# Performance work log

Hardware: AMD Instinct MI355X
Metric: run time of the kernel (lower is better)

Reference implementation:

```python
import jax, jax.numpy as jnp
import numpy as np

E = 1024  # embed_dim
H = 16    # num_heads
D = E // H  # head_dim
B, S = 2, 2048

def _xavier(key, shape):
    fan_in, fan_out = shape[1], shape[0]
    limit = float(np.sqrt(6.0 / (fan_in + fan_out)))
    return jax.random.uniform(key, shape, jnp.float32, -limit, limit)

def setup_inputs() -> dict:
    key = jax.random.key(0)
    ks = jax.random.split(key, 7)
    return {
        "query": jax.random.normal(ks[0], (B, S, E), jnp.float32),
        "key": jax.random.normal(ks[1], (B, S, E), jnp.float32),
        "value": jax.random.normal(ks[2], (B, S, E), jnp.float32),
        "Wq": _xavier(ks[3], (E, E)), "bq": jnp.zeros((E,), jnp.float32),
        "Wk": _xavier(ks[4], (E, E)), "bk": jnp.zeros((E,), jnp.float32),
        "Wv": _xavier(ks[5], (E, E)), "bv": jnp.zeros((E,), jnp.float32),
        "Wo": _xavier(ks[6], (E, E)), "bo": jnp.zeros((E,), jnp.float32),
    }

def reference(query, key, value, Wq, bq, Wk, bk, Wv, bv, Wo, bo):
    b, s, e = query.shape
    # nn.Linear: x @ W^T + b
    Q = (query @ Wq.T + bq).reshape(b, s, H, D).transpose(0, 2, 1, 3)  # [b,h,s,d]
    K = (key @ Wk.T + bk).reshape(b, s, H, D).transpose(0, 2, 1, 3)
    V = (value @ Wv.T + bv).reshape(b, s, H, D).transpose(0, 2, 1, 3)
    scale = D ** -0.5
    scores = jnp.einsum('bhqd,bhkd->bhqk', Q, K) * scale  # [b,h,s,s]
    attn = jax.nn.softmax(scores, axis=-1)  # dropout=0.0 -> identity
    out = jnp.einsum('bhqk,bhkd->bhqd', attn, V)
    out = out.transpose(0, 2, 1, 3).reshape(b, s, e)
    return out @ Wo.T + bo
```

## Files before the change

### kernel.cpp

```cpp
#include <hip/hip_runtime.h>
#include <stdint.h>

#define E_DIM 1024
#define N_HEADS 16
#define HEAD_D 64
#define BATCH 2
#define SEQ 2048
#define M_ROWS (BATCH*SEQ)

typedef __attribute__((ext_vector_type(8))) short short8;
typedef __attribute__((ext_vector_type(4))) short short4_t;
typedef __attribute__((ext_vector_type(4))) float f32x4;
typedef __attribute__((ext_vector_type(4))) int i32x4;
typedef __attribute__((ext_vector_type(2))) int i32x2;

__device__ __forceinline__ unsigned short f2bf(float f) {
  uint32_t u = __float_as_uint(f);
  u += 0x7FFFu + ((u >> 16) & 1u);
  return (unsigned short)(u >> 16);
}

__device__ __forceinline__ void gload_lds16(const void* g, void* l) {
  __builtin_amdgcn_global_load_lds(
      (const __attribute__((address_space(1))) uint32_t*)(uintptr_t)g,
      (__attribute__((address_space(3))) uint32_t*)(uint32_t)(uintptr_t)l,
      16, 0, 0);
}

__device__ __forceinline__ int cvtpk(float lo, float hi) {
  int r;
  asm("v_cvt_pk_bf16_f32 %0, %1, %2" : "=v"(r) : "v"(lo), "v"(hi));
  return r;
}

__device__ __forceinline__ void cvt_body(const float* __restrict__ src,
                                         unsigned short* __restrict__ dst, int i) {
  f32x4 a = ((const f32x4*)src)[2*i];
  f32x4 b = ((const f32x4*)src)[2*i + 1];
  union { unsigned short us[8]; i32x4 v; } o;
  o.us[0] = f2bf(a[0]); o.us[1] = f2bf(a[1]);
  o.us[2] = f2bf(a[2]); o.us[3] = f2bf(a[3]);
  o.us[4] = f2bf(b[0]); o.us[5] = f2bf(b[1]);
  o.us[6] = f2bf(b[2]); o.us[7] = f2bf(b[3]);
  ((i32x4*)dst)[i] = o.v;
}

__global__ void cvt3_f32_bf16(const float* __restrict__ s0, const float* __restrict__ s1,
                              const float* __restrict__ s2,
                              unsigned short* __restrict__ d0, unsigned short* __restrict__ d1,
                              unsigned short* __restrict__ d2, int n8) {
  int i = blockIdx.x * blockDim.x + threadIdx.x;
  if (i >= n8) return;
  const float* s = (blockIdx.y == 0) ? s0 : (blockIdx.y == 1) ? s1 : s2;
  unsigned short* d = (blockIdx.y == 0) ? d0 : (blockIdx.y == 1) ? d1 : d2;
  cvt_body(s, d, i);
}

__global__ void cvt4_f32_bf16(const float* __restrict__ s0, const float* __restrict__ s1,
                              const float* __restrict__ s2, const float* __restrict__ s3,
                              unsigned short* __restrict__ d0, unsigned short* __restrict__ d1,
                              unsigned short* __restrict__ d2, unsigned short* __restrict__ d3,
                              int n8) {
  int i = blockIdx.x * blockDim.x + threadIdx.x;
  if (i >= n8) return;
  const float* s = (blockIdx.y == 0) ? s0 : (blockIdx.y == 1) ? s1
                 : (blockIdx.y == 2) ? s2 : s3;
  unsigned short* d = (blockIdx.y == 0) ? d0 : (blockIdx.y == 1) ? d1
                    : (blockIdx.y == 2) ? d2 : d3;
  cvt_body(s, d, i);
}

__device__ __forceinline__ void gemm_body_rt(const unsigned short* __restrict__ A,
                                             const unsigned short* __restrict__ Bm,
                                             const float* __restrict__ bias,
                                             unsigned short* __restrict__ Cout,
                                             float scale, int bx, int by,
                                             int Nstr, bool brow) {
  constexpr int BM = 128, BN = 64, BK = 64, K = E_DIM;
  __shared__ __attribute__((aligned(16))) unsigned short Al[2][BM*BK];
  __shared__ __attribute__((aligned(16))) unsigned short Bl[2][BN*BK];
  const int tid  = threadIdx.x;
  const int lane = tid & 63, w = tid >> 6;
  const int wm = w >> 1, wn = w & 1;
  const int l15 = lane & 15, l4 = lane >> 4, l7 = lane & 7;
  const int m0 = by * BM, n0 = bx * BN;
  const int jr = lane >> 3, jc = lane & 7;
  const int kcg = jc ^ jr;

#define GSTAGE(KT, BUF)                                                        \
  do {                                                                         \
    _Pragma("unroll")                                                          \
    for (int t = 0; t < 4; ++t) {             \
      int ia = w*4 + t;                                                        \
      const char* src = (const char*)A +                                       \
          ((size_t)(m0 + ia*8 + jr)*K + (KT))*2 + (kcg << 4);                  \
      gload_lds16(src, (char*)Al[BUF] + ia*1024);                              \
    }                                                                          \
    _Pragma("unroll")                                                          \
    for (int t = 0; t < 2; ++t) {                     \
      int ib = w*2 + t;                                                        \
      const char* src = (const char*)Bm +                                      \
          ((size_t)(n0 + ib*8 + jr)*K + (KT))*2 + (kcg << 4);                  \
      gload_lds16(src, (char*)Bl[BUF] + ib*1024);                              \
    }                                                                          \
  } while (0)

  f32x4 zero = {0.f, 0.f, 0.f, 0.f};
  f32x4 acc[4][2];
  for (int i = 0; i < 4; ++i) for (int j = 0; j < 2; ++j) acc[i][j] = zero;

  GSTAGE(0, 0);
  __syncthreads();

  int cur = 0;
  const int NKT = K / BK;
  for (int kt = 0; kt < NKT; ++kt) {
    if (kt + 1 < NKT) GSTAGE((kt + 1) * BK, cur ^ 1);

#pragma unroll
    for (int ks = 0; ks < 2; ++ks) {
      const int sw = ((ks*4 + l4) ^ l7) << 4;
      short8 af[4], bf[2];
#pragma unroll
      for (int mf = 0; mf < 4; ++mf)
        af[mf] = *(const short8*)((const char*)Al[cur] + (wm*64 + mf*16 + l15)*128 + sw);
#pragma unroll
      for (int nf = 0; nf < 2; ++nf)
        bf[nf] = *(const short8*)((const char*)Bl[cur] + (wn*32 + nf*16 + l15)*128 + sw);
#pragma unroll
      for (int mf = 0; mf < 4; ++mf)
#pragma unroll
        for (int nf = 0; nf < 2; ++nf)
          acc[mf][nf] = __builtin_amdgcn_mfma_f32_16x16x32_bf16(
              af[mf], bf[nf], acc[mf][nf], 0, 0, 0);
    }

    __syncthreads();
    cur ^= 1;
  }
#undef GSTAGE

#pragma unroll
  for (int nf = 0; nf < 2; ++nf) {
    const int col = n0 + wn*32 + nf*16 + l15;
    const float bcol = brow ? 0.f : bias[col];
#pragma unroll
    for (int mf = 0; mf < 4; ++mf) {
      const int rowb = m0 + wm*64 + mf*16 + l4*4;
#pragma unroll
      for (int r = 0; r < 4; ++r) {
        const float bv = brow ? bias[rowb + r] : bcol;
        float v = (acc[mf][nf][r] + bv) * scale;
        Cout[(size_t)(rowb + r)*Nstr + col] = f2bf(v);
      }
    }
  }
}

__global__ __launch_bounds__(256, 2)
void gemm_qkv(const unsigned short* __restrict__ Xq, const unsigned short* __restrict__ Xk,
              const unsigned short* __restrict__ Xv,
              const unsigned short* __restrict__ Wq, const unsigned short* __restrict__ Wk,
              const unsigned short* __restrict__ Wv,
              const float* __restrict__ bq, const float* __restrict__ bk,
              const float* __restrict__ bv,
              unsigned short* __restrict__ Qb, unsigned short* __restrict__ Kb,
              unsigned short* __restrict__ Vt, float scale0) {
  const int z = blockIdx.z;
  const int idx = blockIdx.x;
  if (z == 2) {
    gemm_body_rt(Wv, Xv, bv, Vt, 1.0f, idx & 63, idx >> 6, M_ROWS, true);
  } else {
    const unsigned short* A  = (z == 0) ? Xq : Xk;
    const unsigned short* Bm = (z == 0) ? Wq : Wk;
    const float* bias        = (z == 0) ? bq : bk;
    unsigned short* C        = (z == 0) ? Qb : Kb;
    const float scale        = (z == 0) ? scale0 : 1.0f;
    gemm_body_rt(A, Bm, bias, C, scale, idx & 15, idx >> 4, E_DIM, false);
  }
}

__global__ __launch_bounds__(256, 2)
void gemm_o(const unsigned short* __restrict__ A, const unsigned short* __restrict__ Bm,
            const float* __restrict__ bias, float* __restrict__ Cout) {
  constexpr int BM = 128, BN = 64, BK = 64, K = E_DIM, N = E_DIM;
  __shared__ __attribute__((aligned(16))) unsigned short Al[2][BM*BK];
  __shared__ __attribute__((aligned(16))) unsigned short Bl[2][BN*BK];
  const int tid  = threadIdx.x;
  const int lane = tid & 63, w = tid >> 6;
  const int wm = w >> 1, wn = w & 1;
  const int l15 = lane & 15, l4 = lane >> 4, l7 = lane & 7;
  const int m0 = blockIdx.y * BM, n0 = blockIdx.x * BN;
  const int jr = lane >> 3, jc = lane & 7;
  const int kcg = jc ^ jr;

#define GSTAGE(KT, BUF)                                                        \
  do {                                                                         \
    _Pragma("unroll")                                                          \
    for (int t = 0; t < 4; ++t) {                                              \
      int ia = w*4 + t;                                                        \
      const char* src = (const char*)A +                                       \
          ((size_t)(m0 + ia*8 + jr)*K + (KT))*2 + (kcg << 4);                  \
      gload_lds16(src, (char*)Al[BUF] + ia*1024);                              \
    }                                                                          \
    _Pragma("unroll")                                                          \
    for (int t = 0; t < 2; ++t) {                                              \
      int ib = w*2 + t;                                                        \
      const char* src = (const char*)Bm +                                      \
          ((size_t)(n0 + ib*8 + jr)*K + (KT))*2 + (kcg << 4);                  \
      gload_lds16(src, (char*)Bl[BUF] + ib*1024);                              \
    }                                                                          \
  } while (0)

  f32x4 zero = {0.f, 0.f, 0.f, 0.f};
  f32x4 acc[4][2];
  for (int i = 0; i < 4; ++i) for (int j = 0; j < 2; ++j) acc[i][j] = zero;

  GSTAGE(0, 0);
  __syncthreads();

  int cur = 0;
  const int NKT = K / BK;
  for (int kt = 0; kt < NKT; ++kt) {
    if (kt + 1 < NKT) GSTAGE((kt + 1) * BK, cur ^ 1);
#pragma unroll
    for (int ks = 0; ks < 2; ++ks) {
      const int sw = ((ks*4 + l4) ^ l7) << 4;
      short8 af[4], bf[2];
#pragma unroll
      for (int mf = 0; mf < 4; ++mf)
        af[mf] = *(const short8*)((const char*)Al[cur] + (wm*64 + mf*16 + l15)*128 + sw);
#pragma unroll
      for (int nf = 0; nf < 2; ++nf)
        bf[nf] = *(const short8*)((const char*)Bl[cur] + (wn*32 + nf*16 + l15)*128 + sw);
#pragma unroll
      for (int mf = 0; mf < 4; ++mf)
#pragma unroll
        for (int nf = 0; nf < 2; ++nf)
          acc[mf][nf] = __builtin_amdgcn_mfma_f32_16x16x32_bf16(
              af[mf], bf[nf], acc[mf][nf], 0, 0, 0);
    }
    __syncthreads();
    cur ^= 1;
  }
#undef GSTAGE

#pragma unroll
  for (int nf = 0; nf < 2; ++nf) {
    const int col = n0 + wn*32 + nf*16 + l15;
    const float bv = bias[col];
#pragma unroll
    for (int mf = 0; mf < 4; ++mf) {
      const int rowb = m0 + wm*64 + mf*16 + l4*4;
#pragma unroll
      for (int r = 0; r < 4; ++r)
        Cout[(size_t)(rowb + r)*N + col] = acc[mf][nf][r] + bv;
    }
  }
}

__global__ __launch_bounds__(512, 2)
void attn_fwd6(const unsigned short* __restrict__ Q,
               const unsigned short* __restrict__ Kg,
               const unsigned short* __restrict__ Vt_g,
               unsigned short* __restrict__ O) {
  __shared__ __attribute__((aligned(16))) unsigned short Kl[2][4096];
  __shared__ __attribute__((aligned(16))) unsigned short Vl[2][4096];
  __shared__ __attribute__((aligned(16))) unsigned short Pl[8][1024];

  const int tid = threadIdx.x;
  const int l = tid & 63, w = tid >> 6;
  const int l15 = l & 15, l4 = l >> 4, l7 = l & 7;

  const int id = blockIdx.x;
  const int bh = (id & 7) * 4 + ((id >> 3) & 3);
  const int qt = id >> 5;
  const int b = bh >> 4, h = bh & 15;
  const size_t bS = (size_t)b * SEQ;
  const int qw = qt * 128 + w * 16;

  short8 qf[2];
  {
    const char* qp = (const char*)Q + ((bS + qw + l15) * E_DIM + h * 64) * 2;
    qf[0] = *(const short8*)(qp + l4 * 16);
    qf[1] = *(const short8*)(qp + 64 + l4 * 16);
  }

  f32x4 zero = {0.f, 0.f, 0.f, 0.f};
  f32x4 oacc[4];
#pragma unroll
  for (int i = 0; i < 4; ++i) oacc[i] = zero;
  float mrow = -1e30f, lrow = 0.f;

  const int krow = l >> 3;
  const int kcg  = (l & 7) ^ krow;
  const char* vt_base = (const char*)Vt_g +
      ((size_t)(h * 64 + 8 * w + krow) * M_ROWS + bS) * 2 + (kcg << 4);

#define KSTAGE(KT, BUF)                                                        \
  gload_lds16((const char*)Kg +                                                \
                  ((bS + (size_t)(KT)*64 + 8*w + krow) * E_DIM + h*64 + kcg*8)*2, \
              (char*)Kl[BUF] + w * 1024)

#define VSTAGE(KT, BUF)                                                        \
  gload_lds16(vt_base + (size_t)(KT) * 128, (char*)Vl[BUF] + w * 1024)

  KSTAGE(0, 0);
  VSTAGE(0, 0);
  __syncthreads();

  int cur = 0;
  constexpr int NT = SEQ / 64;
  for (int kt = 0; kt < NT; ++kt) {
    const bool more = (kt + 1 < NT);
    if (more) {
      KSTAGE(kt + 1, cur ^ 1);
      VSTAGE(kt + 1, cur ^ 1);
    }

    f32x4 s[4];
    const char* kb = (const char*)Kl[cur];
#pragma unroll
    for (int nf = 0; nf < 4; ++nf) {
      const char* rowb = kb + (nf * 16 + l15) * 128;
      short8 k0 = *(const short8*)(rowb + ((l4 ^ l7) << 4));
      short8 k1 = *(const short8*)(rowb + (((4 + l4) ^ l7) << 4));
      f32x4 z = zero;
      z = __builtin_amdgcn_mfma_f32_16x16x32_bf16(k0, qf[0], z, 0, 0, 0);
      z = __builtin_amdgcn_mfma_f32_16x16x32_bf16(k1, qf[1], z, 0, 0, 0);
      s[nf] = z;
    }

    float mx = s[0][0];
#pragma unroll
    for (int nf = 0; nf < 4; ++nf)
#pragma unroll
      for (int r = 0; r < 4; ++r) mx = fmaxf(mx, s[nf][r]);
    mx = fmaxf(mx, __shfl_xor(mx, 16));
    mx = fmaxf(mx, __shfl_xor(mx, 32));
    const float mnew = fmaxf(mrow, mx);
    const float fac = __builtin_amdgcn_exp2f(mrow - mnew);
    mrow = mnew;

    float pv[4][4];
    float rs = 0.f;
#pragma unroll
    for (int nf = 0; nf < 4; ++nf)
#pragma unroll
      for (int r = 0; r < 4; ++r) {
        float p = __builtin_amdgcn_exp2f(s[nf][r] - mnew);
        pv[nf][r] = p;
        rs += p;
      }
    rs += __shfl_xor(rs, 16);
    rs += __shfl_xor(rs, 32);
    lrow = lrow * fac + rs;

    unsigned short* pw = Pl[w];
#pragma unroll
    for (int nf = 0; nf < 4; ++nf) {
      const int c = nf * 2 + (l4 >> 1);
      i32x2 pk;
      pk.x = cvtpk(pv[nf][0], pv[nf][1]);
      pk.y = cvtpk(pv[nf][2], pv[nf][3]);
      *(i32x2*)((char*)pw + l15 * 128 + ((c ^ l7) << 4) + ((l4 & 1) << 3)) = pk;
    }
    short8 pf0 = *(const short8*)((const char*)pw + l15 * 128 + ((l4 ^ l7) << 4));
    short8 pf1 = *(const short8*)((const char*)pw + l15 * 128 + (((4 + l4) ^ l7) << 4));

#pragma unroll
    for (int df = 0; df < 4; ++df)
#pragma unroll
      for (int r = 0; r < 4; ++r) oacc[df][r] *= fac;

    const char* vb = (const char*)Vl[cur];
#pragma unroll
    for (int df = 0; df < 4; ++df) {
      const char* rowb = vb + (df * 16 + l15) * 128;
      short8 v0 = *(const short8*)(rowb + ((l4 ^ l7) << 4));
      short8 v1 = *(const short8*)(rowb + (((4 + l4) ^ l7) << 4));
      oacc[df] = __builtin_amdgcn_mfma_f32_16x16x32_bf16(v0, pf0, oacc[df], 0, 0, 0);
      oacc[df] = __builtin_amdgcn_mfma_f32_16x16x32_bf16(v1, pf1, oacc[df], 0, 0, 0);
    }

    __syncthreads();
    cur ^= 1;
  }
#undef KSTAGE
#undef VSTAGE

  const float rinv = __builtin_amdgcn_rcpf(lrow);
  unsigned short* orow = O + (bS + qw + l15) * E_DIM + h * 64;
#pragma unroll
  for (int df = 0; df < 4; ++df) {
    short4_t o4;
#pragma unroll
    for (int r = 0; r < 4; ++r) o4[r] = (short)f2bf(oacc[df][r] * rinv);
    *(short4_t*)(orow + df * 16 + l4 * 4) = o4;
  }
}

extern "C" void kernel_launch(void* const* d_in, const int* in_sizes, int n_in,
                              void* d_out, int out_size, void* d_ws, size_t ws_size,
                              hipStream_t stream) {
  const float* q_in = (const float*)d_in[0];
  const float* k_in = (const float*)d_in[1];
  const float* v_in = (const float*)d_in[2];
  const float* Wq = (const float*)d_in[3];
  const float* bq = (const float*)d_in[4];
  const float* Wk = (const float*)d_in[5];
  const float* bk = (const float*)d_in[6];
  const float* Wv = (const float*)d_in[7];
  const float* bv = (const float*)d_in[8];
  const float* Wo = (const float*)d_in[9];
  const float* bo = (const float*)d_in[10];

  char* ws = (char*)d_ws;
  const size_t XB = (size_t)M_ROWS * E_DIM * 2;
  const size_t WB = (size_t)E_DIM * E_DIM * 2;
  unsigned short* Xq  = (unsigned short*)(ws);
  unsigned short* Xk  = (unsigned short*)(ws + XB);
  unsigned short* Xv  = (unsigned short*)(ws + 2*XB);
  unsigned short* Wqb = (unsigned short*)(ws + 3*XB);
  unsigned short* Wkb = (unsigned short*)(ws + 3*XB + WB);
  unsigned short* Wvb = (unsigned short*)(ws + 3*XB + 2*WB);
  unsigned short* Wob = (unsigned short*)(ws + 3*XB + 3*WB);
  unsigned short* Qb  = (unsigned short*)(ws + 3*XB + 4*WB);
  unsigned short* Kb  = (unsigned short*)(ws + 4*XB + 4*WB);
  unsigned short* Vtg = (unsigned short*)(ws + 5*XB + 4*WB);
  unsigned short* Ob  = (unsigned short*)(ws + 6*XB + 4*WB);

  const int nX8 = M_ROWS * E_DIM / 8;
  const int nW8 = E_DIM * E_DIM / 8;
  cvt3_f32_bf16<<<dim3(nX8/256, 3), 256, 0, stream>>>(q_in, k_in, v_in, Xq, Xk, Xv, nX8);
  cvt4_f32_bf16<<<dim3(nW8/256, 4), 256, 0, stream>>>(Wq, Wk, Wv, Wo, Wqb, Wkb, Wvb, Wob, nW8);

  const float qscale = 0.125f * 1.44269504088896340736f;
  gemm_qkv<<<dim3(512, 1, 3), 256, 0, stream>>>(Xq, Xk, Xv, Wqb, Wkb, Wvb,
                                                bq, bk, bv, Qb, Kb, Vtg, qscale);

  attn_fwd6<<<512, 512, 0, stream>>>(Qb, Kb, Vtg, Ob);

  dim3 ogrid(E_DIM/64, M_ROWS/128);
  gemm_o<<<ogrid, 256, 0, stream>>>(Ob, Wob, bo, (float*)d_out);
}
```

Measured before the change: 123.4 us.

## Enlarge QKV GEMM tile to 128x128, merge conversion kernels, add MFMA priority hints

The QKV projection GEMM now uses 128x128 tiles computed by 512-thread blocks (8 waves in a 2x4 grid), which halves the block count and raises operand reuse per LDS tile. The two f32-to-bf16 conversion kernels are merged into one launch covering activations and weights. s_setprio raises wave priority around the MFMA sequences in the GEMMs and the attention kernel, so matrix work is favoured over other waves' issue. The larger tile uses more LDS per block and the 512-thread launch bound may limit registers and occupancy.

```diff
diff --git a/kernel.cpp b/kernel.cpp
--- a/kernel.cpp
+++ b/kernel.cpp
@@ -45,43 +45,43 @@
   ((i32x4*)dst)[i] = o.v;
 }
 
-__global__ void cvt3_f32_bf16(const float* __restrict__ s0, const float* __restrict__ s1,
-                              const float* __restrict__ s2,
-                              unsigned short* __restrict__ d0, unsigned short* __restrict__ d1,
-                              unsigned short* __restrict__ d2, int n8) {
-  int i = blockIdx.x * blockDim.x + threadIdx.x;
-  if (i >= n8) return;
-  const float* s = (blockIdx.y == 0) ? s0 : (blockIdx.y == 1) ? s1 : s2;
-  unsigned short* d = (blockIdx.y == 0) ? d0 : (blockIdx.y == 1) ? d1 : d2;
-  cvt_body(s, d, i);
-}
-
-__global__ void cvt4_f32_bf16(const float* __restrict__ s0, const float* __restrict__ s1,
-                              const float* __restrict__ s2, const float* __restrict__ s3,
-                              unsigned short* __restrict__ d0, unsigned short* __restrict__ d1,
-                              unsigned short* __restrict__ d2, unsigned short* __restrict__ d3,
-                              int n8) {
-  int i = blockIdx.x * blockDim.x + threadIdx.x;
-  if (i >= n8) return;
-  const float* s = (blockIdx.y == 0) ? s0 : (blockIdx.y == 1) ? s1
-                 : (blockIdx.y == 2) ? s2 : s3;
-  unsigned short* d = (blockIdx.y == 0) ? d0 : (blockIdx.y == 1) ? d1
-                    : (blockIdx.y == 2) ? d2 : d3;
-  cvt_body(s, d, i);
-}
-
-__device__ __forceinline__ void gemm_body_rt(const unsigned short* __restrict__ A,
-                                             const unsigned short* __restrict__ Bm,
-                                             const float* __restrict__ bias,
-                                             unsigned short* __restrict__ Cout,
-                                             float scale, int bx, int by,
-                                             int Nstr, bool brow) {
-  constexpr int BM = 128, BN = 64, BK = 64, K = E_DIM;
+__global__ void cvt_all(const float* __restrict__ x0, const float* __restrict__ x1,
+                        const float* __restrict__ x2,
+                        const float* __restrict__ w0, const float* __restrict__ w1,
+                        const float* __restrict__ w2, const float* __restrict__ w3,
+                        unsigned short* __restrict__ dx0, unsigned short* __restrict__ dx1,
+                        unsigned short* __restrict__ dx2,
+                        unsigned short* __restrict__ dw0, unsigned short* __restrict__ dw1,
+                        unsigned short* __restrict__ dw2, unsigned short* __restrict__ dw3) {
+  const int i = blockIdx.x * blockDim.x + threadIdx.x;
+  constexpr int NX8 = M_ROWS * E_DIM / 8;
+  constexpr int NW8 = E_DIM * E_DIM / 8;
+  if (i < 3 * NX8) {
+    const int r = i >> 19, off = i & (NX8 - 1);
+    const float* s = (r == 0) ? x0 : (r == 1) ? x1 : x2;
+    unsigned short* d = (r == 0) ? dx0 : (r == 1) ? dx1 : dx2;
+    cvt_body(s, d, off);
+  } else {
+    const int j = i - 3 * NX8;
+    const int r = j >> 17, off = j & (NW8 - 1);
+    const float* s = (r == 0) ? w0 : (r == 1) ? w1 : (r == 2) ? w2 : w3;
+    unsigned short* d = (r == 0) ? dw0 : (r == 1) ? dw1 : (r == 2) ? dw2 : dw3;
+    cvt_body(s, d, off);
+  }
+}
+
+__device__ __forceinline__ void gemm_body_rt8(const unsigned short* __restrict__ A,
+                                              const unsigned short* __restrict__ Bm,
+                                              const float* __restrict__ bias,
+                                              unsigned short* __restrict__ Cout,
+                                              float scale, int bx, int by,
+                                              int Nstr, bool brow) {
+  constexpr int BM = 128, BN = 128, BK = 64, K = E_DIM;
   __shared__ __attribute__((aligned(16))) unsigned short Al[2][BM*BK];
   __shared__ __attribute__((aligned(16))) unsigned short Bl[2][BN*BK];
   const int tid  = threadIdx.x;
   const int lane = tid & 63, w = tid >> 6;
-  const int wm = w >> 1, wn = w & 1;
+  const int wm = w >> 2, wn = w & 3;
   const int l15 = lane & 15, l4 = lane >> 4, l7 = lane & 7;
   const int m0 = by * BM, n0 = bx * BN;
   const int jr = lane >> 3, jc = lane & 7;
@@ -90,14 +90,14 @@
 #define GSTAGE(KT, BUF)                                                        \
   do {                                                                         \
     _Pragma("unroll")                                                          \
-    for (int t = 0; t < 4; ++t) {             \
-      int ia = w*4 + t;                                                        \
+    for (int t = 0; t < 2; ++t) {             \
+      int ia = w*2 + t;                                                        \
       const char* src = (const char*)A +                                       \
           ((size_t)(m0 + ia*8 + jr)*K + (KT))*2 + (kcg << 4);                  \
       gload_lds16(src, (char*)Al[BUF] + ia*1024);                              \
     }                                                                          \
     _Pragma("unroll")                                                          \
-    for (int t = 0; t < 2; ++t) {                     \
+    for (int t = 0; t < 2; ++t) {                    \
       int ib = w*2 + t;                                                        \
       const char* src = (const char*)Bm +                                      \
           ((size_t)(n0 + ib*8 + jr)*K + (KT))*2 + (kcg << 4);                  \
@@ -127,12 +127,14 @@
 #pragma unroll
       for (int nf = 0; nf < 2; ++nf)
         bf[nf] = *(const short8*)((const char*)Bl[cur] + (wn*32 + nf*16 + l15)*128 + sw);
+      __builtin_amdgcn_s_setprio(1);
 #pragma unroll
       for (int mf = 0; mf < 4; ++mf)
 #pragma unroll
         for (int nf = 0; nf < 2; ++nf)
           acc[mf][nf] = __builtin_amdgcn_mfma_f32_16x16x32_bf16(
               af[mf], bf[nf], acc[mf][nf], 0, 0, 0);
+      __builtin_amdgcn_s_setprio(0);
     }
 
     __syncthreads();
@@ -157,7 +159,7 @@
   }
 }
 
-__global__ __launch_bounds__(256, 2)
+__global__ __launch_bounds__(512, 4)
 void gemm_qkv(const unsigned short* __restrict__ Xq, const unsigned short* __restrict__ Xk,
               const unsigned short* __restrict__ Xv,
               const unsigned short* __restrict__ Wq, const unsigned short* __restrict__ Wk,
@@ -169,14 +171,14 @@
   const int z = blockIdx.z;
   const int idx = blockIdx.x;
   if (z == 2) {
-    gemm_body_rt(Wv, Xv, bv, Vt, 1.0f, idx & 63, idx >> 6, M_ROWS, true);
+    gemm_body_rt8(Wv, Xv, bv, Vt, 1.0f, idx & 31, idx >> 5, M_ROWS, true);
   } else {
     const unsigned short* A  = (z == 0) ? Xq : Xk;
     const unsigned short* Bm = (z == 0) ? Wq : Wk;
     const float* bias        = (z == 0) ? bq : bk;
     unsigned short* C        = (z == 0) ? Qb : Kb;
     const float scale        = (z == 0) ? scale0 : 1.0f;
-    gemm_body_rt(A, Bm, bias, C, scale, idx & 15, idx >> 4, E_DIM, false);
+    gemm_body_rt8(A, Bm, bias, C, scale, idx & 7, idx >> 3, E_DIM, false);
   }
 }
 
@@ -233,12 +235,14 @@
 #pragma unroll
       for (int nf = 0; nf < 2; ++nf)
         bf[nf] = *(const short8*)((const char*)Bl[cur] + (wn*32 + nf*16 + l15)*128 + sw);
+      __builtin_amdgcn_s_setprio(1);
 #pragma unroll
       for (int mf = 0; mf < 4; ++mf)
 #pragma unroll
         for (int nf = 0; nf < 2; ++nf)
           acc[mf][nf] = __builtin_amdgcn_mfma_f32_16x16x32_bf16(
               af[mf], bf[nf], acc[mf][nf], 0, 0, 0);
+      __builtin_amdgcn_s_setprio(0);
     }
     __syncthreads();
     cur ^= 1;
@@ -320,6 +324,7 @@
 
     f32x4 s[4];
     const char* kb = (const char*)Kl[cur];
+    __builtin_amdgcn_s_setprio(1);
 #pragma unroll
     for (int nf = 0; nf < 4; ++nf) {
       const char* rowb = kb + (nf * 16 + l15) * 128;
@@ -330,6 +335,7 @@
       z = __builtin_amdgcn_mfma_f32_16x16x32_bf16(k1, qf[1], z, 0, 0, 0);
       s[nf] = z;
     }
+    __builtin_amdgcn_s_setprio(0);
 
     float mx = s[0][0];
 #pragma unroll
@@ -374,6 +380,7 @@
       for (int r = 0; r < 4; ++r) oacc[df][r] *= fac;
 
     const char* vb = (const char*)Vl[cur];
+    __builtin_amdgcn_s_setprio(1);
 #pragma unroll
     for (int df = 0; df < 4; ++df) {
       const char* rowb = vb + (df * 16 + l15) * 128;
@@ -382,6 +389,7 @@
       oacc[df] = __builtin_amdgcn_mfma_f32_16x16x32_bf16(v0, pf0, oacc[df], 0, 0, 0);
       oacc[df] = __builtin_amdgcn_mfma_f32_16x16x32_bf16(v1, pf1, oacc[df], 0, 0, 0);
     }
+    __builtin_amdgcn_s_setprio(0);
 
     __syncthreads();
     cur ^= 1;
@@ -430,13 +438,11 @@
   unsigned short* Vtg = (unsigned short*)(ws + 5*XB + 4*WB);
   unsigned short* Ob  = (unsigned short*)(ws + 6*XB + 4*WB);
 
-  const int nX8 = M_ROWS * E_DIM / 8;
-  const int nW8 = E_DIM * E_DIM / 8;
-  cvt3_f32_bf16<<<dim3(nX8/256, 3), 256, 0, stream>>>(q_in, k_in, v_in, Xq, Xk, Xv, nX8);
-  cvt4_f32_bf16<<<dim3(nW8/256, 4), 256, 0, stream>>>(Wq, Wk, Wv, Wo, Wqb, Wkb, Wvb, Wob, nW8);
+  cvt_all<<<8192, 256, 0, stream>>>(q_in, k_in, v_in, Wq, Wk, Wv, Wo,
+                                    Xq, Xk, Xv, Wqb, Wkb, Wvb, Wob);
 
   const float qscale = 0.125f * 1.44269504088896340736f;
-  gemm_qkv<<<dim3(512, 1, 3), 256, 0, stream>>>(Xq, Xk, Xv, Wqb, Wkb, Wvb,
+  gemm_qkv<<<dim3(256, 1, 3), 512, 0, stream>>>(Xq, Xk, Xv, Wqb, Wkb, Wvb,
                                                 bq, bk, bv, Qb, Kb, Vtg, qscale);
 
   attn_fwd6<<<512, 512, 0, stream>>>(Qb, Kb, Vtg, Ob);
```

Result: no change. 122.3 us (-0.9%).
